# Performance work log

Measured on AMD Instinct MI355X. Metric: run time of the kernel, lower is better.

Reference implementation:

```python
import jax, jax.numpy as jnp
import numpy as np

V = 196608      # HEALPix nside=128 vertices
DEG = 9         # nnz per row (8 neighbors + self)
C = 64          # in_channels == out_channels
K = 8           # Chebyshev kernel_size
B = 1
EPS = 1e-5


def setup_inputs() -> dict:
    key = jax.random.key(0)
    ks = jax.random.split(key, 8)
    nnz = V * DEG
    x = jax.random.normal(ks[0], (B, V, C), dtype=jnp.float32)
    lap_rows = jnp.repeat(jnp.arange(V, dtype=jnp.int64), DEG)
    lap_cols = jax.random.randint(ks[1], (nnz,), 0, V, dtype=jnp.int64)
    lap_vals = jax.random.normal(ks[2], (nnz,), dtype=jnp.float32) * 0.1
    gamma = jnp.ones((C,), dtype=jnp.float32)
    beta = jnp.zeros((C,), dtype=jnp.float32)
    # Chebyshev weight [K, Fin, Fout], kaiming-like scale
    weight = jax.random.normal(ks[3], (K, C, C), dtype=jnp.float32) * (1.0 / np.sqrt(C * K))
    bias = jnp.zeros((C,), dtype=jnp.float32)
    return {"x": x, "lap_rows": lap_rows, "lap_cols": lap_cols, "lap_vals": lap_vals,
            "gamma": gamma, "beta": beta, "weight": weight, "bias": bias}


def _mish(h):
    return h * jnp.tanh(jax.nn.softplus(h))


def reference(x, lap_rows, lap_cols, lap_vals, gamma, beta, weight, bias):
    Bb, Vv, Cc = x.shape
    Kk = weight.shape[0]
    # BatchNorm1d (training-mode batch stats) over (B, V) per channel
    mean = jnp.mean(x, axis=(0, 1))
    var = jnp.var(x, axis=(0, 1))
    h = (x - mean) * jax.lax.rsqrt(var + EPS) * gamma + beta
    # Mish activation
    h = _mish(h)
    # Chebyshev spectral conv: x_k = 2*L@x_{k-1} - x_{k-2}
    def lap_mm(y):  # y: [V, M] sparse L @ y via gather + segment-sum scatter
        return jax.ops.segment_sum(lap_vals[:, None] * y[lap_cols], lap_rows,
                                   num_segments=Vv)
    x0 = jnp.transpose(h, (1, 0, 2)).reshape(Vv, Bb * Cc)  # [V, B*Fin]
    xs = [x0]
    if Kk > 1:
        xs.append(lap_mm(x0))
    for _ in range(2, Kk):
        xs.append(2.0 * lap_mm(xs[-1]) - xs[-2])
    Xk = jnp.stack(xs, axis=0).reshape(Kk, Vv, Bb, Cc)  # [K, V, B, Fin]
    out = jnp.einsum('kvbi,kio->bvo', Xk, weight) + bias  # [B, V, Fout]
    return out
```

## Files before the change

### kernel.cpp

```cpp
#include <hip/hip_runtime.h>
#include <math.h>

#define NV 196608
#define NDEG 9
#define NC 64
#define NK 8
#define TILE 64
#define NBLK (NV / TILE)
#define SLOT ((size_t)NV * NC)
static constexpr float EPS = 1e-5f;

typedef __attribute__((ext_vector_type(8))) short bf16x8;
typedef __attribute__((ext_vector_type(4))) short bf16x4;
typedef __attribute__((ext_vector_type(4))) float f32x4;
typedef int   i32x4u __attribute__((ext_vector_type(4), aligned(4)));
typedef float f32x4u __attribute__((ext_vector_type(4), aligned(4)));

__device__ __forceinline__ short f2bf(float f) {
    unsigned u = __float_as_uint(f);
    unsigned r = (u + 0x7fffu + ((u >> 16) & 1u)) >> 16;
    return (short)r;
}
__device__ __forceinline__ float bf2f(short h) {
    return __uint_as_float(((unsigned)(unsigned short)h) << 16);
}

__device__ __forceinline__ float mish_f(float h) {
    float t = __expf(fminf(h, 20.f));
    float p = 1.f + t;
    float p2 = p * p;
    return h * ((p2 - 1.f) / (p2 + 1.f));
}

#define LDSOFF(r, c) ((r) * 64 + (((c) ^ ((r) & 7)) * 8))

__global__ void __launch_bounds__(256) stats_wconv_kernel(
    const float* __restrict__ x, float* __restrict__ stats,
    const float* __restrict__ w, unsigned short* __restrict__ Wb) {
    if (blockIdx.x >= 1024) {
        int idx = (blockIdx.x - 1024) * 256 + threadIdx.x;
        int i = idx & 63, o = (idx >> 6) & 63, k = idx >> 12;
        Wb[idx] = (unsigned short)f2bf(w[k * 4096 + i * 64 + o]);
        return;
    }
    const float4* x4 = (const float4*)x;
    int t = blockIdx.x * 256 + threadIdx.x;
    int stride = 1024 * 256;
    float4 s = {0.f, 0.f, 0.f, 0.f}, ss = {0.f, 0.f, 0.f, 0.f};
    for (int i = t; i < NV * (NC / 4); i += stride) {
        float4 v = x4[i];
        s.x += v.x; s.y += v.y; s.z += v.z; s.w += v.w;
        ss.x += v.x * v.x; ss.y += v.y * v.y; ss.z += v.z * v.z; ss.w += v.w * v.w;
    }
    __shared__ float4 ls[256], lss[256];
    ls[threadIdx.x] = s;
    lss[threadIdx.x] = ss;
    __syncthreads();
    if (threadIdx.x < 64) {
        int ch = threadIdx.x;
        int g = ch >> 2, comp = ch & 3;
        float a = 0.f, b = 0.f;
        #pragma unroll
        for (int k = 0; k < 16; ++k) {
            float4 v1 = ls[k * 16 + g];
            float4 v2 = lss[k * 16 + g];
            a += (comp == 0) ? v1.x : (comp == 1) ? v1.y : (comp == 2) ? v1.z : v1.w;
            b += (comp == 0) ? v2.x : (comp == 1) ? v2.y : (comp == 2) ? v2.z : v2.w;
        }
        atomicAdd(&stats[ch], a);
        atomicAdd(&stats[64 + ch], b);
    }
}

__global__ void __launch_bounds__(256) bn_mish_k0(
    const float* __restrict__ x, const float* __restrict__ stats,
    const float* __restrict__ gamma, const float* __restrict__ beta,
    unsigned short* __restrict__ dst) {
    int lane = threadIdx.x & 63;
    int wave = threadIdx.x >> 6;
    int c4 = lane & 15, rg = lane >> 4;
    int tile0 = blockIdx.x * TILE;

    float4 sc, sh;
    {
        float4 su = ((const float4*)stats)[c4];
        float4 sq = ((const float4*)stats)[16 + c4];
        float4 g4 = ((const float4*)gamma)[c4];
        float4 b4 = ((const float4*)beta)[c4];
        #define BNC(comp) { float mu = su.comp * (1.f / NV);                     \
                            float va = sq.comp * (1.f / NV) - mu * mu;           \
                            float rs = rsqrtf(va + EPS);                         \
                            sc.comp = g4.comp * rs;                              \
                            sh.comp = b4.comp - mu * sc.comp; }
        BNC(x) BNC(y) BNC(z) BNC(w)
        #undef BNC
    }

    const float4* x4 = (const float4*)x;
    #pragma unroll
    for (int it = 0; it < 4; ++it) {
        int v = tile0 + wave * 16 + it * 4 + rg;
        float4 h = x4[v * 16 + c4];
        float4 m;
        m.x = mish_f(h.x * sc.x + sh.x);
        m.y = mish_f(h.y * sc.y + sh.y);
        m.z = mish_f(h.z * sc.z + sh.z);
        m.w = mish_f(h.w * sc.w + sh.w);
        bf16x4 xb = { f2bf(m.x), f2bf(m.y), f2bf(m.z), f2bf(m.w) };
        *(bf16x4*)(dst + (size_t)v * NC + 4 * c4) = xb;
    }
}

template <bool FIRST>
__global__ void __launch_bounds__(256) cheb_step(
    const int* __restrict__ cols, const float* __restrict__ vals,
    const unsigned short* __restrict__ src, const unsigned short* __restrict__ prev,
    unsigned short* __restrict__ dst) {
    int lane = threadIdx.x & 63;
    int wave = threadIdx.x >> 6;
    int c8 = lane & 7, rg = lane >> 3;
    int tile0 = blockIdx.x * TILE;

    #pragma unroll
    for (int it = 0; it < 2; ++it) {
        int v = tile0 + wave * 16 + it * 8 + rg;
        const int* cp = cols + v * NDEG;
        const float* vp = vals + v * NDEG;
        i32x4u c03 = *(const i32x4u*)cp;
        i32x4u c47 = *(const i32x4u*)(cp + 4);
        int    cl8 = cp[8];
        f32x4u a03 = *(const f32x4u*)vp;
        f32x4u a47 = *(const f32x4u*)(vp + 4);
        float  al8 = vp[8];

        int   cj[NDEG] = { c03[0], c03[1], c03[2], c03[3],
                           c47[0], c47[1], c47[2], c47[3], cl8 };
        float aj[NDEG] = { a03[0], a03[1], a03[2], a03[3],
                           a47[0], a47[1], a47[2], a47[3], al8 };

        bf16x8 g[NDEG];
        #pragma unroll
        for (int j = 0; j < NDEG; ++j)
            g[j] = *(const bf16x8*)(src + (size_t)cj[j] * NC + c8 * 8);

        float s[8] = {0.f, 0.f, 0.f, 0.f, 0.f, 0.f, 0.f, 0.f};
        #pragma unroll
        for (int j = 0; j < NDEG; ++j)
            #pragma unroll
            for (int q = 0; q < 8; ++q) s[q] += aj[j] * bf2f(g[j][q]);

        bf16x8 xb;
        if (FIRST) {
            #pragma unroll
            for (int q = 0; q < 8; ++q) xb[q] = f2bf(s[q]);
        } else {
            bf16x8 p = __builtin_nontemporal_load(
                           (const bf16x8*)(prev + (size_t)v * NC + c8 * 8));
            #pragma unroll
            for (int q = 0; q < 8; ++q) xb[q] = f2bf(2.f * s[q] - bf2f(p[q]));
        }
        *(bf16x8*)(dst + (size_t)v * NC + c8 * 8) = xb;
    }
}

__global__ void __launch_bounds__(256) gemm_all(
    const unsigned short* __restrict__ basis, const unsigned short* __restrict__ Wb,
    const float* __restrict__ bias, float* __restrict__ out) {
    __shared__ short Al[2][NC * NC];
    __shared__ short Wl[2][NC * NC];

    const int tid  = threadIdx.x;
    const int lane = tid & 63;
    const int wave = tid >> 6;
    const int m16  = lane & 15, qq = lane >> 4;
    const int tile0 = blockIdx.x * TILE;

    const int rA = tid >> 3, cA = tid & 7;

    bf16x8 pa0, pa1, pw0, pw1;
    {
        const unsigned short* bp = basis + (size_t)(tile0 + rA) * NC + cA * 8;
        pa0 = __builtin_nontemporal_load((const bf16x8*)bp);
        pa1 = __builtin_nontemporal_load((const bf16x8*)(bp + 32 * NC));
        pw0 = *(const bf16x8*)(Wb + rA * NC + cA * 8);
        pw1 = *(const bf16x8*)(Wb + (rA + 32) * NC + cA * 8);
        *(bf16x8*)&Al[0][LDSOFF(rA, cA)] = pa0;
        *(bf16x8*)&Al[0][LDSOFF(rA + 32, cA)] = pa1;
        *(bf16x8*)&Wl[0][LDSOFF(rA, cA)] = pw0;
        *(bf16x8*)&Wl[0][LDSOFF(rA + 32, cA)] = pw1;
    }
    __syncthreads();

    f32x4 acc[4];
    #pragma unroll
    for (int nt = 0; nt < 4; ++nt) acc[nt] = (f32x4){0.f, 0.f, 0.f, 0.f};

    #pragma unroll
    for (int k = 0; k < NK; ++k) {
        if (k + 1 < NK) {
            const unsigned short* bp =
                basis + (size_t)(k + 1) * SLOT + (size_t)(tile0 + rA) * NC + cA * 8;
            pa0 = __builtin_nontemporal_load((const bf16x8*)bp);
            pa1 = __builtin_nontemporal_load((const bf16x8*)(bp + 32 * NC));
            const unsigned short* wp = Wb + (k + 1) * NC * NC;
            pw0 = *(const bf16x8*)(wp + rA * NC + cA * 8);
            pw1 = *(const bf16x8*)(wp + (rA + 32) * NC + cA * 8);
        }
        const short* ab = Al[k & 1];
        const short* wb = Wl[k & 1];
        bf16x8 a0 = *(const bf16x8*)&ab[LDSOFF(wave * 16 + m16, qq)];
        bf16x8 a1 = *(const bf16x8*)&ab[LDSOFF(wave * 16 + m16, qq + 4)];
        #pragma unroll
        for (int nt = 0; nt < 4; ++nt) {
            int o = nt * 16 + m16;
            bf16x8 b0 = *(const bf16x8*)&wb[LDSOFF(o, qq)];
            bf16x8 b1 = *(const bf16x8*)&wb[LDSOFF(o, qq + 4)];
            acc[nt] = __builtin_amdgcn_mfma_f32_16x16x32_bf16(a0, b0, acc[nt], 0, 0, 0);
            acc[nt] = __builtin_amdgcn_mfma_f32_16x16x32_bf16(a1, b1, acc[nt], 0, 0, 0);
        }
        if (k + 1 < NK) {
            short* an = Al[(k + 1) & 1];
            short* wn = Wl[(k + 1) & 1];
            *(bf16x8*)&an[LDSOFF(rA, cA)] = pa0;
            *(bf16x8*)&an[LDSOFF(rA + 32, cA)] = pa1;
            *(bf16x8*)&wn[LDSOFF(rA, cA)] = pw0;
            *(bf16x8*)&wn[LDSOFF(rA + 32, cA)] = pw1;
            __syncthreads();
        }
    }

    #pragma unroll
    for (int nt = 0; nt < 4; ++nt) {
        float bcol = bias[nt * 16 + m16];
        #pragma unroll
        for (int r = 0; r < 4; ++r) {
            int vout = tile0 + wave * 16 + qq * 4 + r;
            out[(size_t)vout * NC + nt * 16 + m16] = acc[nt][r] + bcol;
        }
    }
}

__global__ void __launch_bounds__(256) gemm_bases(
    const unsigned short* __restrict__ basis, const unsigned short* __restrict__ Wb,
    const float* __restrict__ bias, float* __restrict__ out,
    int kb, int kc, int S, int first) {
    int lane = threadIdx.x & 63;
    int wave = threadIdx.x >> 6;
    int m16 = lane & 15, qq = lane >> 4;
    int tile0 = blockIdx.x * TILE;

    f32x4 acc[4];
    #pragma unroll
    for (int nt = 0; nt < 4; ++nt) acc[nt] = (f32x4){0.f, 0.f, 0.f, 0.f};

    #pragma unroll 1
    for (int j = 0; j < kc; ++j) {
        int k = kb + j;
        const unsigned short* bs =
            basis + (size_t)(k % S) * SLOT + (size_t)(tile0 + wave * 16 + m16) * NC;
        bf16x8 a0 = *(const bf16x8*)(bs + qq * 8);
        bf16x8 a1 = *(const bf16x8*)(bs + 32 + qq * 8);
        const unsigned short* wk = Wb + (size_t)k * NC * NC;
        #pragma unroll
        for (int nt = 0; nt < 4; ++nt) {
            const unsigned short* wr = wk + (nt * 16 + m16) * NC;
            bf16x8 b0 = *(const bf16x8*)(wr + qq * 8);
            bf16x8 b1 = *(const bf16x8*)(wr + 32 + qq * 8);
            acc[nt] = __builtin_amdgcn_mfma_f32_16x16x32_bf16(a0, b0, acc[nt], 0, 0, 0);
            acc[nt] = __builtin_amdgcn_mfma_f32_16x16x32_bf16(a1, b1, acc[nt], 0, 0, 0);
        }
    }

    #pragma unroll
    for (int nt = 0; nt < 4; ++nt) {
        float bcol = bias[nt * 16 + m16];
        #pragma unroll
        for (int r = 0; r < 4; ++r) {
            int vout = tile0 + wave * 16 + qq * 4 + r;
            float* po = out + (size_t)vout * NC + nt * 16 + m16;
            *po = first ? (acc[nt][r] + bcol) : (*po + acc[nt][r]);
        }
    }
}

extern "C" void kernel_launch(void* const* d_in, const int* in_sizes, int n_in,
                              void* d_out, int out_size, void* d_ws, size_t ws_size,
                              hipStream_t stream) {
    const float* x      = (const float*)d_in[0];
    const int*   cols   = (const int*)  d_in[2];
    const float* vals   = (const float*)d_in[3];
    const float* gamma  = (const float*)d_in[4];
    const float* beta   = (const float*)d_in[5];
    const float* weight = (const float*)d_in[6];
    const float* bias   = (const float*)d_in[7];
    float* out = (float*)d_out;

    char* wsb = (char*)d_ws;
    float*          stats = (float*)wsb;
    unsigned short* Wb    = (unsigned short*)(wsb + 1024);
    unsigned short* basis = (unsigned short*)(wsb + 131072);

    int S = (int)((ws_size - 131072) / (SLOT * sizeof(unsigned short)));
    if (S > NK) S = NK;
    if (S < 3) S = 3;

    hipMemsetAsync(stats, 0, 1024, stream);
    stats_wconv_kernel<<<1152, 256, 0, stream>>>(x, stats, weight, Wb);
    bn_mish_k0<<<NBLK, 256, 0, stream>>>(x, stats, gamma, beta, basis);

    if (S >= NK) {
        for (int k = 1; k < NK; ++k) {
            const unsigned short* src = basis + (size_t)(k - 1) * SLOT;
            unsigned short*       dst = basis + (size_t)k * SLOT;
            if (k == 1) {
                cheb_step<true><<<NBLK, 256, 0, stream>>>(cols, vals, src, src, dst);
            } else {
                const unsigned short* prev = basis + (size_t)(k - 2) * SLOT;
                cheb_step<false><<<NBLK, 256, 0, stream>>>(cols, vals, src, prev, dst);
            }
        }
        gemm_all<<<NBLK, 256, 0, stream>>>(basis, Wb, bias, out);
    } else {
        int kb = 0, gsize = S, first = 1;
        while (kb < NK) {
            int kc = (gsize < NK - kb) ? gsize : (NK - kb);
            for (int k = (kb == 0 ? 1 : kb); k < kb + kc; ++k) {
                const unsigned short* src = basis + (size_t)((k - 1) % S) * SLOT;
                unsigned short*       dst = basis + (size_t)(k % S) * SLOT;
                if (k == 1) {
                    cheb_step<true><<<NBLK, 256, 0, stream>>>(cols, vals, src, src, dst);
                } else {
                    const unsigned short* prev = basis + (size_t)((k - 2) % S) * SLOT;
                    cheb_step<false><<<NBLK, 256, 0, stream>>>(cols, vals, src, prev, dst);
                }
            }
            gemm_bases<<<NBLK, 256, 0, stream>>>(basis, Wb, bias, out, kb, kc, S, first);
            first = 0;
            kb += kc;
            gsize = S - 2;
        }
    }
}
```

Measured before the change: 448.1 us.

## Fuse final Chebyshev step into the GEMM kernel, keeping the last basis in LDS

The last Chebyshev recurrence step (k=7) is now computed inside the GEMM kernel per 64-row tile and written straight to shared memory instead of to a global basis slot. This drops one kernel launch plus a full write and read of the last basis (V*64 bf16) through global memory. In exchange the GEMM kernel takes an extra 8 KB of LDS and does a latency-bound gather up front, which may reduce occupancy. The workspace slot requirement for the fast path drops from 8 to 7.

```diff
diff --git a/kernel.cpp b/kernel.cpp
--- a/kernel.cpp
+++ b/kernel.cpp
@@ -163,18 +163,20 @@
     }
 }
 
-__global__ void __launch_bounds__(256) gemm_all(
+__global__ void __launch_bounds__(256) cheb7_gemm(
+    const int* __restrict__ cols, const float* __restrict__ vals,
     const unsigned short* __restrict__ basis, const unsigned short* __restrict__ Wb,
     const float* __restrict__ bias, float* __restrict__ out) {
-    __shared__ short Al[2][NC * NC];
-    __shared__ short Wl[2][NC * NC];
+    __shared__ __align__(16) short Al[2][NC * NC];
+    __shared__ __align__(16) short Wl[2][NC * NC];
+    __shared__ __align__(16) short X7[NC * NC];
 
     const int tid  = threadIdx.x;
     const int lane = tid & 63;
     const int wave = tid >> 6;
-    const int m16  = lane & 15, qq = lane >> 4;
+    const int c8 = lane & 7, rg = lane >> 3;
+    const int m16 = lane & 15, qq = lane >> 4;
     const int tile0 = blockIdx.x * TILE;
-
     const int rA = tid >> 3, cA = tid & 7;
 
     bf16x8 pa0, pa1, pw0, pw1;
@@ -184,11 +186,52 @@
         pa1 = __builtin_nontemporal_load((const bf16x8*)(bp + 32 * NC));
         pw0 = *(const bf16x8*)(Wb + rA * NC + cA * 8);
         pw1 = *(const bf16x8*)(Wb + (rA + 32) * NC + cA * 8);
-        *(bf16x8*)&Al[0][LDSOFF(rA, cA)] = pa0;
-        *(bf16x8*)&Al[0][LDSOFF(rA + 32, cA)] = pa1;
-        *(bf16x8*)&Wl[0][LDSOFF(rA, cA)] = pw0;
-        *(bf16x8*)&Wl[0][LDSOFF(rA + 32, cA)] = pw1;
-    }
+    }
+
+    {
+        const unsigned short* src = basis + (size_t)6 * SLOT;
+        const unsigned short* prv = basis + (size_t)5 * SLOT;
+        #pragma unroll
+        for (int it = 0; it < 2; ++it) {
+            int r = wave * 16 + it * 8 + rg;
+            int v = tile0 + r;
+            const int* cp = cols + v * NDEG;
+            const float* vp = vals + v * NDEG;
+            i32x4u c03 = *(const i32x4u*)cp;
+            i32x4u c47 = *(const i32x4u*)(cp + 4);
+            int    cl8 = cp[8];
+            f32x4u a03 = *(const f32x4u*)vp;
+            f32x4u a47 = *(const f32x4u*)(vp + 4);
+            float  al8 = vp[8];
+
+            int   cj[NDEG] = { c03[0], c03[1], c03[2], c03[3],
+                               c47[0], c47[1], c47[2], c47[3], cl8 };
+            float aj[NDEG] = { a03[0], a03[1], a03[2], a03[3],
+                               a47[0], a47[1], a47[2], a47[3], al8 };
+
+            bf16x8 g[NDEG];
+            #pragma unroll
+            for (int j = 0; j < NDEG; ++j)
+                g[j] = *(const bf16x8*)(src + (size_t)cj[j] * NC + c8 * 8);
+
+            float s[8] = {0.f, 0.f, 0.f, 0.f, 0.f, 0.f, 0.f, 0.f};
+            #pragma unroll
+            for (int j = 0; j < NDEG; ++j)
+                #pragma unroll
+                for (int q = 0; q < 8; ++q) s[q] += aj[j] * bf2f(g[j][q]);
+
+            bf16x8 p = *(const bf16x8*)(prv + (size_t)v * NC + c8 * 8);
+            bf16x8 xb;
+            #pragma unroll
+            for (int q = 0; q < 8; ++q) xb[q] = f2bf(2.f * s[q] - bf2f(p[q]));
+            *(bf16x8*)&X7[LDSOFF(r, c8)] = xb;
+        }
+    }
+
+    *(bf16x8*)&Al[0][LDSOFF(rA, cA)] = pa0;
+    *(bf16x8*)&Al[0][LDSOFF(rA + 32, cA)] = pa1;
+    *(bf16x8*)&Wl[0][LDSOFF(rA, cA)] = pw0;
+    *(bf16x8*)&Wl[0][LDSOFF(rA + 32, cA)] = pw1;
     __syncthreads();
 
     f32x4 acc[4];
@@ -198,15 +241,17 @@
     #pragma unroll
     for (int k = 0; k < NK; ++k) {
         if (k + 1 < NK) {
-            const unsigned short* bp =
-                basis + (size_t)(k + 1) * SLOT + (size_t)(tile0 + rA) * NC + cA * 8;
-            pa0 = __builtin_nontemporal_load((const bf16x8*)bp);
-            pa1 = __builtin_nontemporal_load((const bf16x8*)(bp + 32 * NC));
+            if (k + 1 < NK - 1) {
+                const unsigned short* bp =
+                    basis + (size_t)(k + 1) * SLOT + (size_t)(tile0 + rA) * NC + cA * 8;
+                pa0 = __builtin_nontemporal_load((const bf16x8*)bp);
+                pa1 = __builtin_nontemporal_load((const bf16x8*)(bp + 32 * NC));
+            }
             const unsigned short* wp = Wb + (k + 1) * NC * NC;
             pw0 = *(const bf16x8*)(wp + rA * NC + cA * 8);
             pw1 = *(const bf16x8*)(wp + (rA + 32) * NC + cA * 8);
         }
-        const short* ab = Al[k & 1];
+        const short* ab = (k < NK - 1) ? Al[k & 1] : X7;
         const short* wb = Wl[k & 1];
         bf16x8 a0 = *(const bf16x8*)&ab[LDSOFF(wave * 16 + m16, qq)];
         bf16x8 a1 = *(const bf16x8*)&ab[LDSOFF(wave * 16 + m16, qq + 4)];
@@ -219,10 +264,12 @@
             acc[nt] = __builtin_amdgcn_mfma_f32_16x16x32_bf16(a1, b1, acc[nt], 0, 0, 0);
         }
         if (k + 1 < NK) {
-            short* an = Al[(k + 1) & 1];
+            if (k + 1 < NK - 1) {
+                short* an = Al[(k + 1) & 1];
+                *(bf16x8*)&an[LDSOFF(rA, cA)] = pa0;
+                *(bf16x8*)&an[LDSOFF(rA + 32, cA)] = pa1;
+            }
             short* wn = Wl[(k + 1) & 1];
-            *(bf16x8*)&an[LDSOFF(rA, cA)] = pa0;
-            *(bf16x8*)&an[LDSOFF(rA + 32, cA)] = pa1;
             *(bf16x8*)&wn[LDSOFF(rA, cA)] = pw0;
             *(bf16x8*)&wn[LDSOFF(rA + 32, cA)] = pw1;
             __syncthreads();
@@ -300,7 +347,8 @@
     unsigned short* Wb    = (unsigned short*)(wsb + 1024);
     unsigned short* basis = (unsigned short*)(wsb + 131072);
 
-    int S = (int)((ws_size - 131072) / (SLOT * sizeof(unsigned short)));
+    long long Sll = ((long long)ws_size - 131072) / (long long)(SLOT * sizeof(unsigned short));
+    int S = (Sll < 0) ? 0 : (int)Sll;
     if (S > NK) S = NK;
     if (S < 3) S = 3;
 
@@ -308,8 +356,8 @@
     stats_wconv_kernel<<<1152, 256, 0, stream>>>(x, stats, weight, Wb);
     bn_mish_k0<<<NBLK, 256, 0, stream>>>(x, stats, gamma, beta, basis);
 
-    if (S >= NK) {
-        for (int k = 1; k < NK; ++k) {
+    if (S >= 7) {
+        for (int k = 1; k < NK - 1; ++k) {
             const unsigned short* src = basis + (size_t)(k - 1) * SLOT;
             unsigned short*       dst = basis + (size_t)k * SLOT;
             if (k == 1) {
@@ -319,7 +367,7 @@
                 cheb_step<false><<<NBLK, 256, 0, stream>>>(cols, vals, src, prev, dst);
             }
         }
-        gemm_all<<<NBLK, 256, 0, stream>>>(basis, Wb, bias, out);
+        cheb7_gemm<<<NBLK, 256, 0, stream>>>(cols, vals, basis, Wb, bias, out);
     } else {
         int kb = 0, gsize = S, first = 1;
         while (kb < NK) {
```

Measured after the change: 443.9 us. No clear change (-0.9%).
